# Optimization experiments

Hardware: AMD Instinct MI355X
Metric: run time of the kernel (lower is better)

## Reference

```python
import jax, jax.numpy as jnp
import numpy as np


def setup_inputs() -> dict:
    key = jax.random.key(0)
    B, S, K = 4, 4096, 64
    attn_scores = jax.random.normal(key, (B, S, S), dtype=jnp.float32)
    return {"attn_scores": attn_scores, "k": K}


def reference(attn_scores, k):
    # attn_scores: [B, S, S]; k: python int
    B, S, _ = attn_scores.shape
    # topk over last dim -> indices [B, S, k]
    _, idx = jax.lax.top_k(attn_scores, k)
    # torch.scatter(newmask, 1, idx, zeros): newmask[b, idx[b,s,j], j] = False
    # for s in range(S), j in range(k) (only first k columns are written).
    mask = jnp.ones((B, S, S), dtype=bool)
    b = jnp.arange(B)[:, None, None]      # [B,1,1]
    j = jnp.arange(k)[None, None, :]      # [1,1,k]
    mask = mask.at[b, idx, j].set(False)  # scatter False along row dim
    # triangular overwrite: for i in range(k+1): mask[:, i, i+1:] = True
    rows = jnp.arange(S)[:, None]         # [S,1]
    cols = jnp.arange(S)[None, :]         # [1,S]
    tri = (rows < (k + 1)) & (cols > rows)  # [S,S]
    mask = jnp.where(tri[None, :, :], True, mask)
    return mask[:, None, :, :]            # [B,1,S,S]
```

## Files before the change

### kernel.cpp

```cpp
#include <hip/hip_runtime.h>
#include <stdint.h>

#define S_DIM 4096
#define K_TOP 64
#define THREADS 256
#define EPT 16
#define CAND_CAP 256

__global__ __launch_bounds__(256) void fill_ones_kernel(int4* __restrict__ out, int n4) {
    int i = blockIdx.x * blockDim.x + threadIdx.x;
    const int stride = gridDim.x * blockDim.x;
    const int4 v = make_int4(1, 1, 1, 1);
    for (; i < n4; i += stride) out[i] = v;
}

__device__ __forceinline__ unsigned long long shfl_xor_u64(unsigned long long v, int m) {
    uint32_t lo = (uint32_t)v, hi = (uint32_t)(v >> 32);
    lo = __shfl_xor(lo, m, 64);
    hi = __shfl_xor(hi, m, 64);
    return ((unsigned long long)hi << 32) | lo;
}

__global__ __launch_bounds__(256) void topk_scatter_kernel(const float* __restrict__ scores,
                                                           int* __restrict__ out) {
    const int row  = blockIdx.x;
    const int b    = row >> 12;
    const int t    = threadIdx.x;
    const int lane = t & 63;
    const int wid  = t >> 6;

    __shared__ uint32_t sh_w16[4];
    __shared__ unsigned long long cand[CAND_CAP];
    __shared__ uint32_t sh_count;
    __shared__ unsigned long long sh_wbest[4];
    __shared__ unsigned long long sh_best;

    const float4* rowp = (const float4*)(scores + (size_t)row * S_DIM);
    uint32_t key[EPT];
    #pragma unroll
    for (int i = 0; i < 4; ++i) {
        float4 v = rowp[i * THREADS + t];
        float f[4] = {v.x, v.y, v.z, v.w};
        #pragma unroll
        for (int c = 0; c < 4; ++c) {
            uint32_t ub = __float_as_uint(f[c]);
            key[i * 4 + c] = (ub & 0x80000000u) ? ~ub : (ub | 0x80000000u);
        }
    }

    if (t == 0) sh_count = 0u;

    uint32_t mx = key[0];
    #pragma unroll
    for (int i = 1; i < EPT; ++i) mx = max(mx, key[i]);

    uint32_t x = mx;
    #pragma unroll
    for (int k = 2; k <= 64; k <<= 1) {
        #pragma unroll
        for (int j = k >> 1; j > 0; j >>= 1) {
            uint32_t v = __shfl_xor(x, j, 64);
            bool keepMin = (((lane & j) == 0) == ((lane & k) == 0));
            x = keepMin ? min(x, v) : max(x, v);
        }
    }
    uint32_t w16 = __shfl(x, 48, 64);
    if (lane == 0) sh_w16[wid] = w16;
    __syncthreads();

    const uint32_t Tc = min(min(sh_w16[0], sh_w16[1]), min(sh_w16[2], sh_w16[3]));

    #pragma unroll
    for (int i = 0; i < EPT; ++i) {
        if (key[i] >= Tc) {
            uint32_t idx = (((uint32_t)(i >> 2) * THREADS + (uint32_t)t) << 2) | (uint32_t)(i & 3);
            uint32_t pos = atomicAdd(&sh_count, 1u);
            if (pos < CAND_CAP) {
                cand[pos] = ((unsigned long long)key[i] << 32) | (uint32_t)(~idx);
            }
        }
    }
    __syncthreads();
    const uint32_t m = sh_count;

    if (m <= CAND_CAP) {
        if ((uint32_t)t < m) {
            unsigned long long me = cand[t];
            uint32_t rank = 0;
            for (uint32_t i = 0; i < m; ++i) rank += (cand[i] > me) ? 1u : 0u;
            if (rank < K_TOP) {
                uint32_t idx = ~(uint32_t)me;
                if (idx >= rank) {
                    out[(size_t)b * ((size_t)S_DIM * S_DIM) + (size_t)idx * S_DIM + rank] = 0;
                }
            }
        }
        return;
    }

    uint32_t used = 0u;
    for (int r = 0; r < K_TOP; ++r) {
        unsigned long long best = 0ull;
        #pragma unroll
        for (int i = 0; i < EPT; ++i) {
            if (!(used & (1u << i))) {
                uint32_t idx = (((uint32_t)(i >> 2) * THREADS + (uint32_t)t) << 2) | (uint32_t)(i & 3);
                unsigned long long ck = ((unsigned long long)key[i] << 32) | (uint32_t)(~idx);
                if (ck > best) best = ck;
            }
        }
        #pragma unroll
        for (int off = 32; off > 0; off >>= 1) {
            unsigned long long o = shfl_xor_u64(best, off);
            if (o > best) best = o;
        }
        if (lane == 0) sh_wbest[wid] = best;
        __syncthreads();
        if (t == 0) {
            unsigned long long bb = sh_wbest[0];
            for (int w = 1; w < 4; ++w) if (sh_wbest[w] > bb) bb = sh_wbest[w];
            sh_best = bb;
        }
        __syncthreads();
        const unsigned long long gb = sh_best;
        #pragma unroll
        for (int i = 0; i < EPT; ++i) {
            uint32_t idx = (((uint32_t)(i >> 2) * THREADS + (uint32_t)t) << 2) | (uint32_t)(i & 3);
            unsigned long long ck = ((unsigned long long)key[i] << 32) | (uint32_t)(~idx);
            if (ck == gb) {
                used |= (1u << i);
                uint32_t oidx = ~(uint32_t)gb;
                if (oidx >= (uint32_t)r) {
                    out[(size_t)b * ((size_t)S_DIM * S_DIM) + (size_t)oidx * S_DIM + r] = 0;
                }
            }
        }
        __syncthreads();
    }
}

extern "C" void kernel_launch(void* const* d_in, const int* in_sizes, int n_in,
                              void* d_out, int out_size, void* d_ws, size_t ws_size,
                              hipStream_t stream) {
    const float* scores = (const float*)d_in[0];
    int* out = (int*)d_out;

    const int n4 = out_size / 4;
    hipLaunchKernelGGL(fill_ones_kernel, dim3(2048), dim3(THREADS), 0, stream,
                       (int4*)out, n4);

    const int B = in_sizes[0] / (S_DIM * S_DIM);
    hipLaunchKernelGGL(topk_scatter_kernel, dim3(B * S_DIM), dim3(THREADS), 0, stream,
                       scores, out);
}
```

Baseline: 455.9 us.

## Stage top-k scatter into compact workspace and merge during output fill

The top-k kernel now writes hits into a small [B*S, K] workspace instead of scattering single ints into the 256MB output. A new fill kernel writes the full output once, reading the workspace only for the first K columns and applying the triangular override inline. This removes scattered uncoalesced writes into the big output and the ordering dependency between fill and scatter. In exchange it adds a workspace clear launch and an extra small read pass.

After: 461.0 us. No clear change (+1.1%).

```diff
diff --git a/kernel.cpp b/kernel.cpp
--- a/kernel.cpp
+++ b/kernel.cpp
@@ -7,11 +7,9 @@
 #define EPT 16
 #define CAND_CAP 256
 
-__global__ __launch_bounds__(256) void fill_ones_kernel(int4* __restrict__ out, int n4) {
-    int i = blockIdx.x * blockDim.x + threadIdx.x;
-    const int stride = gridDim.x * blockDim.x;
-    const int4 v = make_int4(1, 1, 1, 1);
-    for (; i < n4; i += stride) out[i] = v;
+
+__global__ __launch_bounds__(256) void clear_zbuf_kernel(int4* __restrict__ zbuf4) {
+    zbuf4[blockIdx.x * blockDim.x + threadIdx.x] = make_int4(0, 0, 0, 0);
 }
 
 __device__ __forceinline__ unsigned long long shfl_xor_u64(unsigned long long v, int m) {
@@ -21,10 +19,9 @@
     return ((unsigned long long)hi << 32) | lo;
 }
 
-__global__ __launch_bounds__(256) void topk_scatter_kernel(const float* __restrict__ scores,
-                                                           int* __restrict__ out) {
+__global__ __launch_bounds__(256) void topk_kernel(const float* __restrict__ scores,
+                                                   int* __restrict__ zbuf) {
     const int row  = blockIdx.x;
-    const int b    = row >> 12;
     const int t    = threadIdx.x;
     const int lane = t & 63;
     const int wid  = t >> 6;
@@ -83,6 +80,8 @@
     __syncthreads();
     const uint32_t m = sh_count;
 
+    const size_t zrow_base = (size_t)row * K_TOP;
+
     if (m <= CAND_CAP) {
         if ((uint32_t)t < m) {
             unsigned long long me = cand[t];
@@ -90,14 +89,14 @@
             for (uint32_t i = 0; i < m; ++i) rank += (cand[i] > me) ? 1u : 0u;
             if (rank < K_TOP) {
                 uint32_t idx = ~(uint32_t)me;
-                if (idx >= rank) {
-                    out[(size_t)b * ((size_t)S_DIM * S_DIM) + (size_t)idx * S_DIM + rank] = 0;
-                }
+                const int b = row >> 12;
+                zbuf[((size_t)((b << 12) | (int)idx)) * K_TOP + rank] = 1;
             }
         }
         return;
     }
 
+    (void)zrow_base;
     uint32_t used = 0u;
     for (int r = 0; r < K_TOP; ++r) {
         unsigned long long best = 0ull;
@@ -130,12 +129,41 @@
             if (ck == gb) {
                 used |= (1u << i);
                 uint32_t oidx = ~(uint32_t)gb;
-                if (oidx >= (uint32_t)r) {
-                    out[(size_t)b * ((size_t)S_DIM * S_DIM) + (size_t)oidx * S_DIM + r] = 0;
-                }
+                const int b = row >> 12;
+                zbuf[((size_t)((b << 12) | (int)oidx)) * K_TOP + r] = 1;
             }
         }
         __syncthreads();
+    }
+}
+
+__global__ __launch_bounds__(256) void fill_merge_kernel(int4* __restrict__ out4,
+                                                         const int4* __restrict__ zbuf4,
+                                                         int n4) {
+    const int stride = gridDim.x * blockDim.x;
+    const int4 ones = make_int4(1, 1, 1, 1);
+    for (int f = blockIdx.x * blockDim.x + threadIdx.x; f < n4; f += stride) {
+        const int c4 = f & 1023;
+        if (c4 >= K_TOP / 4) {
+            out4[f] = ones;
+        } else {
+            const int r = (f >> 10) & (S_DIM - 1);
+            const int b = f >> 22;
+            const int4 z = zbuf4[(size_t)(((b << 12) | r) << 4) + c4];
+            int4 v;
+            v.x = z.x ? 0 : 1;
+            v.y = z.y ? 0 : 1;
+            v.z = z.z ? 0 : 1;
+            v.w = z.w ? 0 : 1;
+            if (r <= K_TOP) {
+                const int c0 = c4 << 2;
+                if (c0 + 0 > r) v.x = 1;
+                if (c0 + 1 > r) v.y = 1;
+                if (c0 + 2 > r) v.z = 1;
+                if (c0 + 3 > r) v.w = 1;
+            }
+            out4[f] = v;
+        }
     }
 }
 
@@ -144,12 +172,18 @@
                               hipStream_t stream) {
     const float* scores = (const float*)d_in[0];
     int* out = (int*)d_out;
+    int* zbuf = (int*)d_ws;
+
+    const int B = in_sizes[0] / (S_DIM * S_DIM);
+
+    const int z4 = B * S_DIM * K_TOP / 4;
+    hipLaunchKernelGGL(clear_zbuf_kernel, dim3(z4 / THREADS), dim3(THREADS), 0, stream,
+                       (int4*)zbuf);
+
+    hipLaunchKernelGGL(topk_kernel, dim3(B * S_DIM), dim3(THREADS), 0, stream,
+                       scores, zbuf);
 
     const int n4 = out_size / 4;
-    hipLaunchKernelGGL(fill_ones_kernel, dim3(2048), dim3(THREADS), 0, stream,
-                       (int4*)out, n4);
-
-    const int B = in_sizes[0] / (S_DIM * S_DIM);
-    hipLaunchKernelGGL(topk_scatter_kernel, dim3(B * S_DIM), dim3(THREADS), 0, stream,
-                       scores, out);
+    hipLaunchKernelGGL(fill_merge_kernel, dim3(8192), dim3(THREADS), 0, stream,
+                       (int4*)out, (const int4*)zbuf, n4);
 }
```
